# Kernel optimization log

Hardware: AMD Instinct MI355X
Metric: run time of the kernel (lower is better)

The kernel has to match this reference:

```python
import jax, jax.numpy as jnp
import numpy as np

B, I, H, O, M = 4096, 1024, 2048, 256, 100


def _lin(key, out_dim, in_dim):
    kw, kb = jax.random.split(key)
    s = 1.0 / np.sqrt(in_dim)
    W = jax.random.uniform(kw, (out_dim, in_dim), jnp.float32, -s, s)
    b = jax.random.uniform(kb, (out_dim,), jnp.float32, -s, s)
    return W, b


def setup_inputs() -> dict:
    key = jax.random.key(0)
    ks = jax.random.split(key, 12)
    W_ch2, b_ch2 = _lin(ks[0], H, I + 3 * H)   # combined_to_hidden2
    W_cm2, b_cm2 = _lin(ks[1], M, I + 3 * H)   # combined_to_middle2
    W_mo, b_mo = _lin(ks[2], O, M)             # middle_to_out
    W_ci, b_ci = _lin(ks[3], H, I)             # linear_cell_i
    W_ch, b_ch = _lin(ks[4], H, H)             # linear_cell_h
    W_fc, b_fc = _lin(ks[5], H, H)             # linear_for_cell
    bias = jax.random.normal(ks[6], (H,), jnp.float32)  # self.bias ~ N(0,1)
    return {
        "input": jax.random.normal(ks[7], (B, I), jnp.float32),
        "hidden": jax.random.normal(ks[8], (B, H), jnp.float32),
        "prev_hidden": jax.random.normal(ks[9], (B, H), jnp.float32),
        "cell": jax.random.normal(ks[10], (B, H), jnp.float32),
        "W_ch2": W_ch2, "b_ch2": b_ch2,
        "W_cm2": W_cm2, "b_cm2": b_cm2,
        "W_mo": W_mo, "b_mo": b_mo,
        "W_ci": W_ci, "b_ci": b_ci,
        "W_ch": W_ch, "b_ch": b_ch,
        "W_fc": W_fc, "b_fc": b_fc,
        "bias": bias,
        "k": 1,
    }


def reference(input, hidden, prev_hidden, cell,
              W_ch2, b_ch2, W_cm2, b_cm2, W_mo, b_mo,
              W_ci, b_ci, W_ch, b_ch, W_fc, b_fc, bias, k):
    # k > 0 branch of TEXTnetOrder2.forward (k is a static Python int)
    assert k != 0
    combined = jnp.concatenate([input, hidden, prev_hidden, cell], axis=1)  # [B, I+3H]
    new_hidden = combined @ W_ch2.T + b_ch2                                  # [B, H]
    mid = jax.nn.relu(combined @ W_cm2.T + b_cm2)                            # [B, 100]
    # dropout(p=0.5) is identity in eval mode
    out = mid @ W_mo.T + b_mo                                                # [B, O]
    h_proj = new_hidden @ W_ch.T + b_ch                                      # linear_cell_h(hidden)
    lc = (input @ W_ci.T + b_ci) + h_proj + bias
    new_cell = jnp.tanh(lc @ W_fc.T + b_fc)      # state update (detached in torch)
    new_prev_hidden = h_proj                      # state update (detached in torch)
    return (out, new_hidden, new_cell, new_prev_hidden)
```

## Files before the change

kernel.cpp:

```cpp
#include <hip/hip_runtime.h>
#include <hip/hip_bf16.h>
#include <math.h>

typedef short bf16x8 __attribute__((ext_vector_type(8)));
typedef float f32x4 __attribute__((ext_vector_type(4)));
typedef unsigned short u16;
typedef unsigned short u16x8v __attribute__((ext_vector_type(8)));

#define DEVI __device__ __forceinline__

DEVI u16 f2b(float x) {
  __hip_bfloat16 h = __float2bfloat16(x);
  return *reinterpret_cast<u16*>(&h);
}

DEVI void load_lds16(const void* g, void* l) {
  __builtin_amdgcn_global_load_lds(
      (__attribute__((address_space(1))) void*)(void*)g,
      (__attribute__((address_space(3))) void*)l, 16, 0, 0);
}

DEVI void gemm_core(const u16* __restrict__ A, int lda,
                    const u16* __restrict__ Bw, int ldb,
                    int K, int m0, int n0,
                    u16* As, u16* Bs, f32x4 (&acc)[4][4])
{
  const int tid = threadIdx.x;
  const int w = tid >> 6, l = tid & 63;
  const int wr = w >> 1, wc = w & 1;
  const int lr = l & 15, kg = l >> 4;
  const int c0 = w * 2;
  const int srow = l >> 2, kq = l & 3;

#pragma unroll
  for (int m = 0; m < 4; ++m)
#pragma unroll
    for (int n = 0; n < 4; ++n) acc[m][n] = (f32x4)0.f;

  int aoff[4], boff[4];
#pragma unroll
  for (int m = 0; m < 4; ++m) {
    int ra = wr * 64 + m * 16 + lr;
    aoff[m] = ra * 32 + ((kg ^ ((ra >> 1) & 3)) << 3);
    int rb = wc * 64 + m * 16 + lr;
    boff[m] = rb * 32 + ((kg ^ ((rb >> 1) & 3)) << 3);
  }

  for (int k0 = 0; k0 < K; k0 += 32) {
    __syncthreads();
#pragma unroll
    for (int i = 0; i < 2; ++i) {
      const int c = c0 + i;
      const int row = c * 16 + srow;
      const int kcol = (kq ^ ((row >> 1) & 3)) << 3;
      load_lds16(A  + (long)(m0 + row) * lda + k0 + kcol, &As[c * 512]);
      load_lds16(Bw + (long)(n0 + row) * ldb + k0 + kcol, &Bs[c * 512]);
    }
    __syncthreads();

    bf16x8 af[4], bfr[4];
#pragma unroll
    for (int m = 0; m < 4; ++m) af[m]  = *reinterpret_cast<const bf16x8*>(&As[aoff[m]]);
#pragma unroll
    for (int n = 0; n < 4; ++n) bfr[n] = *reinterpret_cast<const bf16x8*>(&Bs[boff[n]]);
#pragma unroll
    for (int m = 0; m < 4; ++m)
#pragma unroll
      for (int n = 0; n < 4; ++n)
        acc[m][n] = __builtin_amdgcn_mfma_f32_16x16x32_bf16(af[m], bfr[n], acc[m][n], 0, 0, 0);
  }
}

__global__ __launch_bounds__(256, 2)
void gemmA(const u16* __restrict__ cmb,
           const u16* __restrict__ wch2b, const float* __restrict__ bch2,
           const u16* __restrict__ wcm2b, const float* __restrict__ bcm2,
           const u16* __restrict__ wcib,  const float* __restrict__ bci,
           const float* __restrict__ bias,
           float* __restrict__ out_nh, u16* __restrict__ nhb,
           u16* __restrict__ midb, float* __restrict__ cif)
{
  __shared__ u16 As[128 * 32], Bs[128 * 32];
  const int m0 = blockIdx.y * 128;
  const int bx = blockIdx.x;
  const int tid = threadIdx.x;
  const int w = tid >> 6, l = tid & 63;
  const int wr = w >> 1, wc = w & 1;
  const int lr = l & 15, kg = l >> 4;
  f32x4 acc[4][4];

  if (bx < 16) {
    const int n0 = bx * 128;
    gemm_core(cmb, 7168, wch2b, 7168, 7168, m0, n0, As, Bs, acc);
#pragma unroll
    for (int m = 0; m < 4; ++m) {
      const int r0 = m0 + wr * 64 + m * 16 + kg * 4;
#pragma unroll
      for (int n = 0; n < 4; ++n) {
        const int gc = n0 + wc * 64 + n * 16 + lr;
        const float b1 = bch2[gc];
#pragma unroll
        for (int j = 0; j < 4; ++j) {
          const long idx = (long)(r0 + j) * 2048 + gc;
          float v = acc[m][n][j] + b1;
          out_nh[idx] = v; nhb[idx] = f2b(v);
        }
      }
    }
  } else if (bx == 16) {
    gemm_core(cmb, 7168, wcm2b, 7168, 7168, m0, 0, As, Bs, acc);
#pragma unroll
    for (int m = 0; m < 4; ++m) {
      const int r0 = m0 + wr * 64 + m * 16 + kg * 4;
#pragma unroll
      for (int n = 0; n < 4; ++n) {
        const int gc = wc * 64 + n * 16 + lr;
        const float b1 = (gc < 100) ? bcm2[gc] : 0.0f;
#pragma unroll
        for (int j = 0; j < 4; ++j) {
          float v = acc[m][n][j] + b1;
          midb[(long)(r0 + j) * 128 + gc] = f2b(v > 0.f ? v : 0.f);
        }
      }
    }
  } else {
    const int n0 = (bx - 17) * 128;
    gemm_core(cmb, 7168, wcib, 1024, 1024, m0, n0, As, Bs, acc);
#pragma unroll
    for (int m = 0; m < 4; ++m) {
      const int r0 = m0 + wr * 64 + m * 16 + kg * 4;
#pragma unroll
      for (int n = 0; n < 4; ++n) {
        const int gc = n0 + wc * 64 + n * 16 + lr;
        const float b1 = bci[gc] + bias[gc];
#pragma unroll
        for (int j = 0; j < 4; ++j)
          cif[(long)(r0 + j) * 2048 + gc] = acc[m][n][j] + b1;
      }
    }
  }
}

__global__ __launch_bounds__(256, 2)
void gemmB(const u16* __restrict__ nhb, const u16* __restrict__ wchb,
           const float* __restrict__ bch, const float* __restrict__ cif,
           float* __restrict__ out_ph, u16* __restrict__ lcb,
           const u16* __restrict__ midb, const u16* __restrict__ wmob,
           const float* __restrict__ bmo, float* __restrict__ out_out)
{
  __shared__ u16 As[128 * 32], Bs[128 * 32];
  const int m0 = blockIdx.y * 128;
  const int bx = blockIdx.x;
  const int tid = threadIdx.x;
  const int w = tid >> 6, l = tid & 63;
  const int wr = w >> 1, wc = w & 1;
  const int lr = l & 15, kg = l >> 4;
  f32x4 acc[4][4];

  if (bx < 16) {
    const int n0 = bx * 128;
    gemm_core(nhb, 2048, wchb, 2048, 2048, m0, n0, As, Bs, acc);
#pragma unroll
    for (int m = 0; m < 4; ++m) {
      const int r0 = m0 + wr * 64 + m * 16 + kg * 4;
#pragma unroll
      for (int n = 0; n < 4; ++n) {
        const int gc = n0 + wc * 64 + n * 16 + lr;
        const float b1 = bch[gc];
#pragma unroll
        for (int j = 0; j < 4; ++j) {
          const long idx = (long)(r0 + j) * 2048 + gc;
          float v = acc[m][n][j] + b1;
          out_ph[idx] = v;
          lcb[idx] = f2b(v + cif[idx]);
        }
      }
    }
  } else {
    const int n0 = (bx - 16) * 128;
    gemm_core(midb, 128, wmob, 128, 128, m0, n0, As, Bs, acc);
#pragma unroll
    for (int m = 0; m < 4; ++m) {
      const int r0 = m0 + wr * 64 + m * 16 + kg * 4;
#pragma unroll
      for (int n = 0; n < 4; ++n) {
        const int gc = n0 + wc * 64 + n * 16 + lr;
        const float b1 = bmo[gc];
#pragma unroll
        for (int j = 0; j < 4; ++j)
          out_out[(long)(r0 + j) * 256 + gc] = acc[m][n][j] + b1;
      }
    }
  }
}

__global__ __launch_bounds__(256, 2)
void gemmD(const u16* __restrict__ lcb, const u16* __restrict__ wfcb,
           const float* __restrict__ bfc, float* __restrict__ out_cell)
{
  __shared__ u16 As[128 * 32], Bs[128 * 32];
  const int m0 = blockIdx.y * 128;
  const int n0 = blockIdx.x * 128;
  const int tid = threadIdx.x;
  const int w = tid >> 6, l = tid & 63;
  const int wr = w >> 1, wc = w & 1;
  const int lr = l & 15, kg = l >> 4;
  f32x4 acc[4][4];

  gemm_core(lcb, 2048, wfcb, 2048, 2048, m0, n0, As, Bs, acc);
#pragma unroll
  for (int m = 0; m < 4; ++m) {
    const int r0 = m0 + wr * 64 + m * 16 + kg * 4;
#pragma unroll
    for (int n = 0; n < 4; ++n) {
      const int gc = n0 + wc * 64 + n * 16 + lr;
      const float b1 = bfc[gc];
#pragma unroll
      for (int j = 0; j < 4; ++j)
        out_cell[(long)(r0 + j) * 2048 + gc] = tanhf(acc[m][n][j] + b1);
    }
  }
}

__global__ void cvt_in(const float* __restrict__ x_in, const float* __restrict__ x_hid,
                       const float* __restrict__ x_ph, const float* __restrict__ x_cel,
                       u16* __restrict__ cmb)
{
  const long total = (long)4096 * 896;
  for (long i = blockIdx.x * (long)blockDim.x + threadIdx.x; i < total;
       i += (long)gridDim.x * blockDim.x) {
    const int c8 = (int)(i % 896);
    const long row = i / 896;
    const float* src; long sidx;
    if (c8 < 128)      { src = x_in;  sidx = row * 1024 + (long)c8 * 8; }
    else if (c8 < 384) { src = x_hid; sidx = row * 2048 + (long)(c8 - 128) * 8; }
    else if (c8 < 640) { src = x_ph;  sidx = row * 2048 + (long)(c8 - 384) * 8; }
    else               { src = x_cel; sidx = row * 2048 + (long)(c8 - 640) * 8; }
    float4 v0 = *reinterpret_cast<const float4*>(src + sidx);
    float4 v1 = *reinterpret_cast<const float4*>(src + sidx + 4);
    u16x8v o;
    o[0] = f2b(v0.x); o[1] = f2b(v0.y); o[2] = f2b(v0.z); o[3] = f2b(v0.w);
    o[4] = f2b(v1.x); o[5] = f2b(v1.y); o[6] = f2b(v1.z); o[7] = f2b(v1.w);
    *reinterpret_cast<u16x8v*>(&cmb[row * 7168 + (long)c8 * 8]) = o;
  }
}

__global__ void cvt_w5(const float* __restrict__ s0, const float* __restrict__ s1,
                       const float* __restrict__ s2, const float* __restrict__ s3,
                       const float* __restrict__ s4,
                       u16* __restrict__ d0, u16* __restrict__ d1, u16* __restrict__ d2,
                       u16* __restrict__ d3, u16* __restrict__ d4,
                       long e0, long e1, long e2, long e3, long e4)
{
  for (long i = blockIdx.x * (long)blockDim.x + threadIdx.x; i < e4;
       i += (long)gridDim.x * blockDim.x) {
    const float* s; u16* d; long j;
    if (i < e0)      { s = s0; d = d0; j = i; }
    else if (i < e1) { s = s1; d = d1; j = i - e0; }
    else if (i < e2) { s = s2; d = d2; j = i - e1; }
    else if (i < e3) { s = s3; d = d3; j = i - e2; }
    else             { s = s4; d = d4; j = i - e3; }
    float4 v = reinterpret_cast<const float4*>(s)[j];
    ushort4 o; o.x = f2b(v.x); o.y = f2b(v.y); o.z = f2b(v.z); o.w = f2b(v.w);
    reinterpret_cast<ushort4*>(d)[j] = o;
  }
}

__global__ void cvt_wmo(const float* __restrict__ src, u16* __restrict__ dst)
{
  int i = blockIdx.x * blockDim.x + threadIdx.x;
  if (i < 256 * 100) {
    int r = i / 100, c = i - r * 100;
    dst[r * 128 + c] = f2b(src[i]);
  }
}

extern "C" void kernel_launch(void* const* d_in, const int* in_sizes, int n_in,
                              void* d_out, int out_size, void* d_ws, size_t ws_size,
                              hipStream_t stream) {
  const int B = 4096, I = 1024, H = 2048, O = 256;
  const int K1 = I + 3 * H;

  const float* x_in  = (const float*)d_in[0];
  const float* x_hid = (const float*)d_in[1];
  const float* x_ph  = (const float*)d_in[2];
  const float* x_cel = (const float*)d_in[3];
  const float* Wch2  = (const float*)d_in[4];
  const float* bch2  = (const float*)d_in[5];
  const float* Wcm2  = (const float*)d_in[6];
  const float* bcm2  = (const float*)d_in[7];
  const float* Wmo   = (const float*)d_in[8];
  const float* bmo   = (const float*)d_in[9];
  const float* Wci   = (const float*)d_in[10];
  const float* bci   = (const float*)d_in[11];
  const float* Wch   = (const float*)d_in[12];
  const float* bch   = (const float*)d_in[13];
  const float* Wfc   = (const float*)d_in[14];
  const float* bfc   = (const float*)d_in[15];
  const float* bias  = (const float*)d_in[16];

  float* out_out  = (float*)d_out;
  float* out_nh   = out_out + (long)B * O;
  float* out_cell = out_nh + (long)B * H;
  float* out_ph   = out_cell + (long)B * H;

  char* p = (char*)d_ws;
  u16* cmb   = (u16*)p; p += (long)B * K1 * 2;
  u16* wch2b = (u16*)p; p += (long)H * K1 * 2;
  u16* wcm2b = (u16*)p; p += (long)128 * K1 * 2;
  u16* wmob  = (u16*)p; p += (long)O * 128 * 2;
  u16* wcib  = (u16*)p; p += (long)H * I * 2;
  u16* wchb  = (u16*)p; p += (long)H * H * 2;
  u16* wfcb  = (u16*)p; p += (long)H * H * 2;
  u16* nhb   = (u16*)p; p += (long)B * H * 2;
  u16* midb  = (u16*)p; p += (long)B * 128 * 2;
  u16* lcb   = (u16*)p; p += (long)B * H * 2;

  const dim3 cb(256);

  hipMemsetAsync(wcm2b + (long)100 * K1, 0, (size_t)(28 * K1 + 256 * 128) * 2, stream);

  cvt_in<<<2048, cb, 0, stream>>>(x_in, x_hid, x_ph, x_cel, cmb);
  {
    long e0 = (long)H * K1 / 4;
    long e1 = e0 + (long)100 * K1 / 4;
    long e2 = e1 + (long)H * I / 4;
    long e3 = e2 + (long)H * H / 4;
    long e4 = e3 + (long)H * H / 4;
    cvt_w5<<<2048, cb, 0, stream>>>(Wch2, Wcm2, Wci, Wch, Wfc,
                                    wch2b, wcm2b, wcib, wchb, wfcb,
                                    e0, e1, e2, e3, e4);
  }
  cvt_wmo<<<100, cb, 0, stream>>>(Wmo, wmob);

  gemmA<<<dim3(33, 32), cb, 0, stream>>>(cmb, wch2b, bch2, wcm2b, bcm2,
                                         wcib, bci, bias,
                                         out_nh, nhb, midb, out_cell );
  gemmB<<<dim3(18, 32), cb, 0, stream>>>(nhb, wchb, bch, out_cell ,
                                         out_ph, lcb, midb, wmob, bmo, out_out);
  gemmD<<<dim3(16, 32), cb, 0, stream>>>(lcb, wfcb, bfc, out_cell);

  (void)in_sizes; (void)n_in; (void)out_size; (void)ws_size;
}
```

Before: 442.7 us.

## Use 256x128 tiles with double-buffered LDS pipeline and XCD-aware block swizzle

Replaces the single-buffered 128x128 GEMM core with a 512-thread, 256x128-tile core that stages K=64 per iteration into double-buffered LDS. The next tile's global-to-LDS loads overlap the MFMA work, using explicit waitcnt, barriers, sched fences and setprio. Block IDs are remapped so consecutive blocks on the same XCD share tiles. The aim is to hide memory latency and improve operand reuse, at the cost of 96KB LDS per block and more fragile hand-placed synchronization.

```diff
diff --git a/kernel.cpp b/kernel.cpp
--- a/kernel.cpp
+++ b/kernel.cpp
@@ -8,6 +8,7 @@
 typedef unsigned short u16x8v __attribute__((ext_vector_type(8)));
 
 #define DEVI __device__ __forceinline__
+#define SCHED_FENCE() __builtin_amdgcn_sched_barrier(0)
 
 DEVI u16 f2b(float x) {
   __hip_bfloat16 h = __float2bfloat16(x);
@@ -20,78 +21,122 @@
       (__attribute__((address_space(3))) void*)l, 16, 0, 0);
 }
 
-DEVI void gemm_core(const u16* __restrict__ A, int lda,
-                    const u16* __restrict__ Bw, int ldb,
-                    int K, int m0, int n0,
-                    u16* As, u16* Bs, f32x4 (&acc)[4][4])
+DEVI void gemm8_core(const u16* __restrict__ A, int lda,
+                     const u16* __restrict__ Bw, int ldb,
+                     int nt, int m0, int n0, u16* lds, f32x4 (&acc)[4][4])
 {
   const int tid = threadIdx.x;
-  const int w = tid >> 6, l = tid & 63;
-  const int wr = w >> 1, wc = w & 1;
-  const int lr = l & 15, kg = l >> 4;
-  const int c0 = w * 2;
-  const int srow = l >> 2, kq = l & 3;
+  const int wid = tid >> 6, l = tid & 63;
+  const int wr = wid >> 1, wc = wid & 1;
+  const int lr = l & 15, kg = (l >> 4) & 3;
+
+  const int lq = l & 3, lrow = l >> 2;
+  const int raj0 = (wid * 2 + 0) * 16 + lrow;
+  const int raj1 = (wid * 2 + 1) * 16 + lrow;
+  const int rbw  = wid * 16 + lrow;
+  const int qxA0 = lq ^ ((raj0 >> 1) & 3);
+  const int qxA1 = lq ^ ((raj1 >> 1) & 3);
+  const int qxB  = lq ^ ((rbw  >> 1) & 3);
+  const u16* aSrc0 = A  + (long)(m0 + raj0) * lda + qxA0 * 8;
+  const u16* aSrc1 = A  + (long)(m0 + raj1) * lda + qxA1 * 8;
+  const u16* bSrc  = Bw + (long)(n0 + rbw)  * ldb + qxB  * 8;
+  u16* aDst0 = lds + (wid * 2 + 0) * 512;
+  u16* aDst1 = lds + (wid * 2 + 1) * 512;
+  u16* bDst  = lds + 16384 + wid * 512;
+
+  int aoff[4], boff[4];
+#pragma unroll
+  for (int m = 0; m < 4; ++m) {
+    const int r = wr * 64 + m * 16 + lr;
+    aoff[m] = r * 32 + ((kg ^ ((r >> 1) & 3)) << 3);
+  }
+#pragma unroll
+  for (int n = 0; n < 4; ++n) {
+    const int rb = wc * 64 + n * 16 + lr;
+    boff[n] = 16384 + rb * 32 + ((kg ^ ((rb >> 1) & 3)) << 3);
+  }
 
 #pragma unroll
   for (int m = 0; m < 4; ++m)
 #pragma unroll
     for (int n = 0; n < 4; ++n) acc[m][n] = (f32x4)0.f;
 
-  int aoff[4], boff[4];
-#pragma unroll
-  for (int m = 0; m < 4; ++m) {
-    int ra = wr * 64 + m * 16 + lr;
-    aoff[m] = ra * 32 + ((kg ^ ((ra >> 1) & 3)) << 3);
-    int rb = wc * 64 + m * 16 + lr;
-    boff[m] = rb * 32 + ((kg ^ ((rb >> 1) & 3)) << 3);
-  }
-
-  for (int k0 = 0; k0 < K; k0 += 32) {
-    __syncthreads();
-#pragma unroll
-    for (int i = 0; i < 2; ++i) {
-      const int c = c0 + i;
-      const int row = c * 16 + srow;
-      const int kcol = (kq ^ ((row >> 1) & 3)) << 3;
-      load_lds16(A  + (long)(m0 + row) * lda + k0 + kcol, &As[c * 512]);
-      load_lds16(Bw + (long)(n0 + row) * ldb + k0 + kcol, &Bs[c * 512]);
-    }
-    __syncthreads();
-
-    bf16x8 af[4], bfr[4];
-#pragma unroll
-    for (int m = 0; m < 4; ++m) af[m]  = *reinterpret_cast<const bf16x8*>(&As[aoff[m]]);
-#pragma unroll
-    for (int n = 0; n < 4; ++n) bfr[n] = *reinterpret_cast<const bf16x8*>(&Bs[boff[n]]);
-#pragma unroll
-    for (int m = 0; m < 4; ++m)
+  auto stage = [&](int t, int kh, int s) {
+    const long go = (long)t * 64 + kh * 32;
+    const int  sa = s * 24576 + kh * 8192;
+    const int  sb = s * 24576 + kh * 4096;
+    load_lds16(aSrc0 + go, aDst0 + sa);
+    load_lds16(aSrc1 + go, aDst1 + sa);
+    load_lds16(bSrc  + go, bDst  + sb);
+  };
+
+  stage(0, 0, 0);
+  stage(0, 1, 0);
+  asm volatile("s_waitcnt vmcnt(3)" ::: "memory");
+  SCHED_FENCE();
+  __builtin_amdgcn_s_barrier();
+  SCHED_FENCE();
+
+  int cur = 0;
+  for (int t = 0; t < nt; ++t, cur ^= 1) {
+    const int base = cur * 24576;
+    const bool pre = (t + 1 < nt);
+#pragma unroll
+    for (int ks = 0; ks < 2; ++ks) {
+      bf16x8 af[4], bfr[4];
+#pragma unroll
+      for (int m = 0; m < 4; ++m)
+        af[m] = *reinterpret_cast<const bf16x8*>(&lds[base + ks * 8192 + aoff[m]]);
 #pragma unroll
       for (int n = 0; n < 4; ++n)
-        acc[m][n] = __builtin_amdgcn_mfma_f32_16x16x32_bf16(af[m], bfr[n], acc[m][n], 0, 0, 0);
-  }
-}
-
-__global__ __launch_bounds__(256, 2)
-void gemmA(const u16* __restrict__ cmb,
-           const u16* __restrict__ wch2b, const float* __restrict__ bch2,
-           const u16* __restrict__ wcm2b, const float* __restrict__ bcm2,
-           const u16* __restrict__ wcib,  const float* __restrict__ bci,
-           const float* __restrict__ bias,
-           float* __restrict__ out_nh, u16* __restrict__ nhb,
-           u16* __restrict__ midb, float* __restrict__ cif)
-{
-  __shared__ u16 As[128 * 32], Bs[128 * 32];
-  const int m0 = blockIdx.y * 128;
-  const int bx = blockIdx.x;
-  const int tid = threadIdx.x;
-  const int w = tid >> 6, l = tid & 63;
-  const int wr = w >> 1, wc = w & 1;
-  const int lr = l & 15, kg = l >> 4;
+        bfr[n] = *reinterpret_cast<const bf16x8*>(&lds[base + ks * 4096 + boff[n]]);
+      if (pre) stage(t + 1, ks, cur ^ 1);
+      SCHED_FENCE();
+      __builtin_amdgcn_s_barrier();
+      asm volatile("s_waitcnt lgkmcnt(0)" ::: "memory");
+      SCHED_FENCE();
+      __builtin_amdgcn_s_setprio(1);
+#pragma unroll
+      for (int m = 0; m < 4; ++m)
+#pragma unroll
+        for (int n = 0; n < 4; ++n)
+          acc[m][n] = __builtin_amdgcn_mfma_f32_16x16x32_bf16(af[m], bfr[n], acc[m][n], 0, 0, 0);
+      __builtin_amdgcn_s_setprio(0);
+      SCHED_FENCE();
+      if (pre) asm volatile("s_waitcnt vmcnt(3)" ::: "memory");
+      else     asm volatile("s_waitcnt vmcnt(0)" ::: "memory");
+      __builtin_amdgcn_s_barrier();
+      SCHED_FENCE();
+    }
+  }
+}
+
+#define EPI_SETUP() \
+  const int tid = threadIdx.x; \
+  const int wid = tid >> 6, l = tid & 63; \
+  const int wr = wid >> 1, wc = wid & 1; \
+  const int lr = l & 15, kg = (l >> 4) & 3; (void)lr; (void)kg;
+
+__global__ __launch_bounds__(512, 2)
+void gemm8A(const u16* __restrict__ cmb,
+            const u16* __restrict__ wch2b, const float* __restrict__ bch2,
+            const u16* __restrict__ wcm2b, const float* __restrict__ bcm2,
+            const u16* __restrict__ wcib,  const float* __restrict__ bci,
+            const float* __restrict__ bias,
+            float* __restrict__ out_nh, u16* __restrict__ nhb,
+            u16* __restrict__ midb, float* __restrict__ cif)
+{
+  __shared__ u16 lds[49152];
+  const int id  = blockIdx.x;
+  const int id2 = (id & 7) * 66 + (id >> 3);
+  const int col = id2 >> 4;
+  const int m0  = (id2 & 15) * 256;
+  EPI_SETUP();
   f32x4 acc[4][4];
 
-  if (bx < 16) {
-    const int n0 = bx * 128;
-    gemm_core(cmb, 7168, wch2b, 7168, 7168, m0, n0, As, Bs, acc);
+  if (col < 16) {
+    const int n0 = col * 128;
+    gemm8_core(cmb, 7168, wch2b, 7168, 112, m0, n0, lds, acc);
 #pragma unroll
     for (int m = 0; m < 4; ++m) {
       const int r0 = m0 + wr * 64 + m * 16 + kg * 4;
@@ -107,8 +152,8 @@
         }
       }
     }
-  } else if (bx == 16) {
-    gemm_core(cmb, 7168, wcm2b, 7168, 7168, m0, 0, As, Bs, acc);
+  } else if (col == 16) {
+    gemm8_core(cmb, 7168, wcm2b, 7168, 112, m0, 0, lds, acc);
 #pragma unroll
     for (int m = 0; m < 4; ++m) {
       const int r0 = m0 + wr * 64 + m * 16 + kg * 4;
@@ -124,8 +169,8 @@
       }
     }
   } else {
-    const int n0 = (bx - 17) * 128;
-    gemm_core(cmb, 7168, wcib, 1024, 1024, m0, n0, As, Bs, acc);
+    const int n0 = (col - 17) * 128;
+    gemm8_core(cmb, 7168, wcib, 1024, 16, m0, n0, lds, acc);
 #pragma unroll
     for (int m = 0; m < 4; ++m) {
       const int r0 = m0 + wr * 64 + m * 16 + kg * 4;
@@ -141,25 +186,24 @@
   }
 }
 
-__global__ __launch_bounds__(256, 2)
-void gemmB(const u16* __restrict__ nhb, const u16* __restrict__ wchb,
-           const float* __restrict__ bch, const float* __restrict__ cif,
-           float* __restrict__ out_ph, u16* __restrict__ lcb,
-           const u16* __restrict__ midb, const u16* __restrict__ wmob,
-           const float* __restrict__ bmo, float* __restrict__ out_out)
-{
-  __shared__ u16 As[128 * 32], Bs[128 * 32];
-  const int m0 = blockIdx.y * 128;
-  const int bx = blockIdx.x;
-  const int tid = threadIdx.x;
-  const int w = tid >> 6, l = tid & 63;
-  const int wr = w >> 1, wc = w & 1;
-  const int lr = l & 15, kg = l >> 4;
+__global__ __launch_bounds__(512, 2)
+void gemm8B(const u16* __restrict__ nhb, const u16* __restrict__ wchb,
+            const float* __restrict__ bch, const float* __restrict__ cif,
+            float* __restrict__ out_ph, u16* __restrict__ lcb,
+            const u16* __restrict__ midb, const u16* __restrict__ wmob,
+            const float* __restrict__ bmo, float* __restrict__ out_out)
+{
+  __shared__ u16 lds[49152];
+  const int id  = blockIdx.x;
+  const int id2 = (id & 7) * 36 + (id >> 3);
+  const int col = id2 >> 4;
+  const int m0  = (id2 & 15) * 256;
+  EPI_SETUP();
   f32x4 acc[4][4];
 
-  if (bx < 16) {
-    const int n0 = bx * 128;
-    gemm_core(nhb, 2048, wchb, 2048, 2048, m0, n0, As, Bs, acc);
+  if (col < 16) {
+    const int n0 = col * 128;
+    gemm8_core(nhb, 2048, wchb, 2048, 32, m0, n0, lds, acc);
 #pragma unroll
     for (int m = 0; m < 4; ++m) {
       const int r0 = m0 + wr * 64 + m * 16 + kg * 4;
@@ -177,8 +221,8 @@
       }
     }
   } else {
-    const int n0 = (bx - 16) * 128;
-    gemm_core(midb, 128, wmob, 128, 128, m0, n0, As, Bs, acc);
+    const int n0 = (col - 16) * 128;
+    gemm8_core(midb, 128, wmob, 128, 2, m0, n0, lds, acc);
 #pragma unroll
     for (int m = 0; m < 4; ++m) {
       const int r0 = m0 + wr * 64 + m * 16 + kg * 4;
@@ -194,26 +238,25 @@
   }
 }
 
-__global__ __launch_bounds__(256, 2)
-void gemmD(const u16* __restrict__ lcb, const u16* __restrict__ wfcb,
-           const float* __restrict__ bfc, float* __restrict__ out_cell)
-{
-  __shared__ u16 As[128 * 32], Bs[128 * 32];
-  const int m0 = blockIdx.y * 128;
-  const int n0 = blockIdx.x * 128;
-  const int tid = threadIdx.x;
-  const int w = tid >> 6, l = tid & 63;
-  const int wr = w >> 1, wc = w & 1;
-  const int lr = l & 15, kg = l >> 4;
+__global__ __launch_bounds__(512, 2)
+void gemm8D(const u16* __restrict__ lcb, const u16* __restrict__ wfcb,
+            const float* __restrict__ bfc, float* __restrict__ out_cell)
+{
+  __shared__ u16 lds[49152];
+  const int id  = blockIdx.x;
+  const int id2 = (id & 7) * 32 + (id >> 3);
+  const int col = id2 >> 4;
+  const int m0  = (id2 & 15) * 256;
+  EPI_SETUP();
   f32x4 acc[4][4];
 
-  gemm_core(lcb, 2048, wfcb, 2048, 2048, m0, n0, As, Bs, acc);
+  gemm8_core(lcb, 2048, wfcb, 2048, 32, m0, col * 128, lds, acc);
 #pragma unroll
   for (int m = 0; m < 4; ++m) {
     const int r0 = m0 + wr * 64 + m * 16 + kg * 4;
 #pragma unroll
     for (int n = 0; n < 4; ++n) {
-      const int gc = n0 + wc * 64 + n * 16 + lr;
+      const int gc = col * 128 + wc * 64 + n * 16 + lr;
       const float b1 = bfc[gc];
 #pragma unroll
       for (int j = 0; j < 4; ++j)
@@ -333,12 +376,12 @@
   }
   cvt_wmo<<<100, cb, 0, stream>>>(Wmo, wmob);
 
-  gemmA<<<dim3(33, 32), cb, 0, stream>>>(cmb, wch2b, bch2, wcm2b, bcm2,
-                                         wcib, bci, bias,
-                                         out_nh, nhb, midb, out_cell );
-  gemmB<<<dim3(18, 32), cb, 0, stream>>>(nhb, wchb, bch, out_cell ,
-                                         out_ph, lcb, midb, wmob, bmo, out_out);
-  gemmD<<<dim3(16, 32), cb, 0, stream>>>(lcb, wfcb, bfc, out_cell);
+  gemm8A<<<dim3(528), dim3(512), 0, stream>>>(cmb, wch2b, bch2, wcm2b, bcm2,
+                                              wcib, bci, bias,
+                                              out_nh, nhb, midb, out_cell );
+  gemm8B<<<dim3(288), dim3(512), 0, stream>>>(nhb, wchb, bch, out_cell ,
+                                              out_ph, lcb, midb, wmob, bmo, out_out);
+  gemm8D<<<dim3(256), dim3(512), 0, stream>>>(lcb, wfcb, bfc, out_cell);
 
   (void)in_sizes; (void)n_in; (void)out_size; (void)ws_size;
 }
```

Result: slower. 540.6 us (+22.1%).

## Fuse input-cell GEMM into gemmB accumulator, drop fp32 intermediate buffer

Applied to the files above, without the earlier changes.

The input@W_ci GEMM moves out of gemmA and into gemmB. Since accumulators are no longer zeroed inside gemm_core, gemmB runs it into the same accumulator right after the h_proj GEMM. The summed linear-cell value is written straight to bf16, which removes the fp32 cif write in gemmA and its read back in gemmB. Launch bounds are also raised to 4 blocks per SM to ask for more occupancy, at the risk of register pressure or spills. gemmA loses 16 columns of blocks, and gemmB's heavy blocks now do 1024 extra K iterations, which may unbalance the schedule.

```diff
diff --git a/kernel.cpp b/kernel.cpp
--- a/kernel.cpp
+++ b/kernel.cpp
@@ -32,11 +32,6 @@
   const int c0 = w * 2;
   const int srow = l >> 2, kq = l & 3;
 
-#pragma unroll
-  for (int m = 0; m < 4; ++m)
-#pragma unroll
-    for (int n = 0; n < 4; ++n) acc[m][n] = (f32x4)0.f;
-
   int aoff[4], boff[4];
 #pragma unroll
   for (int m = 0; m < 4; ++m) {
@@ -71,14 +66,16 @@
   }
 }
 
-__global__ __launch_bounds__(256, 2)
+#define ZERO_ACC(acc) \
+  _Pragma("unroll") for (int m = 0; m < 4; ++m) \
+  _Pragma("unroll") for (int n = 0; n < 4; ++n) acc[m][n] = (f32x4)0.f;
+
+__global__ __launch_bounds__(256, 4)
 void gemmA(const u16* __restrict__ cmb,
            const u16* __restrict__ wch2b, const float* __restrict__ bch2,
            const u16* __restrict__ wcm2b, const float* __restrict__ bcm2,
-           const u16* __restrict__ wcib,  const float* __restrict__ bci,
-           const float* __restrict__ bias,
            float* __restrict__ out_nh, u16* __restrict__ nhb,
-           u16* __restrict__ midb, float* __restrict__ cif)
+           u16* __restrict__ midb)
 {
   __shared__ u16 As[128 * 32], Bs[128 * 32];
   const int m0 = blockIdx.y * 128;
@@ -88,6 +85,7 @@
   const int wr = w >> 1, wc = w & 1;
   const int lr = l & 15, kg = l >> 4;
   f32x4 acc[4][4];
+  ZERO_ACC(acc);
 
   if (bx < 16) {
     const int n0 = bx * 128;
@@ -107,7 +105,7 @@
         }
       }
     }
-  } else if (bx == 16) {
+  } else {
     gemm_core(cmb, 7168, wcm2b, 7168, 7168, m0, 0, As, Bs, acc);
 #pragma unroll
     for (int m = 0; m < 4; ++m) {
@@ -123,27 +121,14 @@
         }
       }
     }
-  } else {
-    const int n0 = (bx - 17) * 128;
-    gemm_core(cmb, 7168, wcib, 1024, 1024, m0, n0, As, Bs, acc);
-#pragma unroll
-    for (int m = 0; m < 4; ++m) {
-      const int r0 = m0 + wr * 64 + m * 16 + kg * 4;
-#pragma unroll
-      for (int n = 0; n < 4; ++n) {
-        const int gc = n0 + wc * 64 + n * 16 + lr;
-        const float b1 = bci[gc] + bias[gc];
-#pragma unroll
-        for (int j = 0; j < 4; ++j)
-          cif[(long)(r0 + j) * 2048 + gc] = acc[m][n][j] + b1;
-      }
-    }
-  }
-}
-
-__global__ __launch_bounds__(256, 2)
+  }
+}
+
+__global__ __launch_bounds__(256, 4)
 void gemmB(const u16* __restrict__ nhb, const u16* __restrict__ wchb,
-           const float* __restrict__ bch, const float* __restrict__ cif,
+           const float* __restrict__ bch,
+           const u16* __restrict__ cmb, const u16* __restrict__ wcib,
+           const float* __restrict__ bci, const float* __restrict__ bias,
            float* __restrict__ out_ph, u16* __restrict__ lcb,
            const u16* __restrict__ midb, const u16* __restrict__ wmob,
            const float* __restrict__ bmo, float* __restrict__ out_out)
@@ -156,6 +141,7 @@
   const int wr = w >> 1, wc = w & 1;
   const int lr = l & 15, kg = l >> 4;
   f32x4 acc[4][4];
+  ZERO_ACC(acc);
 
   if (bx < 16) {
     const int n0 = bx * 128;
@@ -168,12 +154,21 @@
         const int gc = n0 + wc * 64 + n * 16 + lr;
         const float b1 = bch[gc];
 #pragma unroll
-        for (int j = 0; j < 4; ++j) {
-          const long idx = (long)(r0 + j) * 2048 + gc;
-          float v = acc[m][n][j] + b1;
-          out_ph[idx] = v;
-          lcb[idx] = f2b(v + cif[idx]);
-        }
+        for (int j = 0; j < 4; ++j)
+          out_ph[(long)(r0 + j) * 2048 + gc] = acc[m][n][j] + b1;
+      }
+    }
+    gemm_core(cmb, 7168, wcib, 1024, 1024, m0, n0, As, Bs, acc);
+#pragma unroll
+    for (int m = 0; m < 4; ++m) {
+      const int r0 = m0 + wr * 64 + m * 16 + kg * 4;
+#pragma unroll
+      for (int n = 0; n < 4; ++n) {
+        const int gc = n0 + wc * 64 + n * 16 + lr;
+        const float b1 = bch[gc] + bci[gc] + bias[gc];
+#pragma unroll
+        for (int j = 0; j < 4; ++j)
+          lcb[(long)(r0 + j) * 2048 + gc] = f2b(acc[m][n][j] + b1);
       }
     }
   } else {
@@ -194,7 +189,7 @@
   }
 }
 
-__global__ __launch_bounds__(256, 2)
+__global__ __launch_bounds__(256, 4)
 void gemmD(const u16* __restrict__ lcb, const u16* __restrict__ wfcb,
            const float* __restrict__ bfc, float* __restrict__ out_cell)
 {
@@ -206,6 +201,7 @@
   const int wr = w >> 1, wc = w & 1;
   const int lr = l & 15, kg = l >> 4;
   f32x4 acc[4][4];
+  ZERO_ACC(acc);
 
   gemm_core(lcb, 2048, wfcb, 2048, 2048, m0, n0, As, Bs, acc);
 #pragma unroll
@@ -333,10 +329,9 @@
   }
   cvt_wmo<<<100, cb, 0, stream>>>(Wmo, wmob);
 
-  gemmA<<<dim3(33, 32), cb, 0, stream>>>(cmb, wch2b, bch2, wcm2b, bcm2,
-                                         wcib, bci, bias,
-                                         out_nh, nhb, midb, out_cell );
-  gemmB<<<dim3(18, 32), cb, 0, stream>>>(nhb, wchb, bch, out_cell ,
+  gemmA<<<dim3(17, 32), cb, 0, stream>>>(cmb, wch2b, bch2, wcm2b, bcm2,
+                                         out_nh, nhb, midb);
+  gemmB<<<dim3(18, 32), cb, 0, stream>>>(nhb, wchb, bch, cmb, wcib, bci, bias,
                                          out_ph, lcb, midb, wmob, bmo, out_out);
   gemmD<<<dim3(16, 32), cb, 0, stream>>>(lcb, wfcb, bfc, out_cell);
 
```

Measured after the change: 411.6 us. 1.08x faster.
